# Performance work log

Measured on AMD Instinct MI355X. Metric: run time of the kernel, lower is better.

The kernel has to match this reference:

```python
import jax, jax.numpy as jnp
import numpy as np

B, T, N, C = 4, 2048, 4, 1024   # batch, seq, expansion_rate, hidden_dim
A = 8                            # max_lora_adapters
SINKHORN_ITERS = 20
EPS = 1e-05


def _logit(x):
    x = jnp.clip(x, 1e-06, 1.0 - 1e-06)
    return jnp.log(x) - jnp.log(1.0 - x)


def setup_inputs() -> dict:
    key = jax.random.key(0)
    ks = jax.random.split(key, 12)
    nC = N * C
    x = jax.random.normal(ks[0], (B, T, N, C), dtype=jnp.float32)
    adapter_indices = jax.random.randint(ks[1], (B,), 0, A)
    # Learned parameters (perturbed from the identity init so gradients are non-trivial)
    input_norm_weight = 1.0 + 0.02 * jax.random.normal(ks[2], (A, nC), dtype=jnp.float32)
    phi_pre = 0.02 * jax.random.normal(ks[3], (A, nC, N), dtype=jnp.float32)
    phi_post = 0.02 * jax.random.normal(ks[4], (A, nC, N), dtype=jnp.float32)
    phi_res = 0.02 * jax.random.normal(ks[5], (A, nC, N * N), dtype=jnp.float32)
    b_pre = _logit(jnp.float32(1.0 / N)) + 0.1 * jax.random.normal(ks[6], (A, N), dtype=jnp.float32)
    b_post = 0.1 * jax.random.normal(ks[7], (A, N), dtype=jnp.float32)
    b_res = 10.0 * jnp.eye(N, dtype=jnp.float32) + jax.random.normal(ks[8], (A, N, N), dtype=jnp.float32)
    alpha_pre = 1.0 + 0.1 * jax.random.normal(ks[9], (A,), dtype=jnp.float32)
    alpha_post = 1.0 + 0.1 * jax.random.normal(ks[10], (A,), dtype=jnp.float32)
    alpha_res = 1.0 + 0.1 * jax.random.normal(ks[11], (A,), dtype=jnp.float32)
    return {
        "x": x,
        "input_norm_weight": input_norm_weight,
        "phi_pre": phi_pre, "phi_post": phi_post, "phi_res": phi_res,
        "b_pre": b_pre, "b_post": b_post, "b_res": b_res,
        "alpha_pre": alpha_pre, "alpha_post": alpha_post, "alpha_res": alpha_res,
        "adapter_indices": adapter_indices,
    }


def _sinkhorn_knopp(M, iters):
    M = jnp.exp(M)
    def step(_, mat):
        mat = mat / mat.sum(axis=-1, keepdims=True)
        mat = mat / mat.sum(axis=-2, keepdims=True)
        return mat
    return jax.lax.fori_loop(0, iters, step, M)


def reference(x, input_norm_weight, phi_pre, phi_post, phi_res,
              b_pre, b_post, b_res, alpha_pre, alpha_post, alpha_res,
              adapter_indices):
    Bb, Tt, n, Cc = x.shape
    idx = adapter_indices.astype(jnp.int32)
    x_flat = x.reshape(Bb, Tt, n * Cc)
    # adapter-indexed RMSNorm
    w = input_norm_weight[idx]                                  # [B, nC]
    rms = jnp.sqrt(jnp.mean(x_flat ** 2, axis=-1, keepdims=True) + EPS)
    x_norm = w[:, None, :] * x_flat / rms                       # [B, T, nC]
    # pre: input-dependent aggregation weights H_pre
    pre_logits = jnp.einsum('btd,bdn->btn', x_norm, phi_pre[idx])
    H_pre = jax.nn.sigmoid(alpha_pre[idx][:, None, None] * pre_logits + b_pre[idx][:, None, :])
    x_agg = (H_pre[..., None] * x).sum(axis=-2)                 # [B, T, C]
    output = x_agg                                              # identity block between pre and post
    # post: distribution weights H_post and doubly-stochastic mixing M
    post_logits = jnp.einsum('btd,bdn->btn', x_norm, phi_post[idx])
    H_post = 2.0 * jax.nn.sigmoid(alpha_post[idx][:, None, None] * post_logits + b_post[idx][:, None, :])
    res_logits = jnp.einsum('btd,bdm->btm', x_norm, phi_res[idx]).reshape(Bb, Tt, n, n)
    tilde_H_res = alpha_res[idx][:, None, None, None] * res_logits + b_res[idx][:, None, :, :]
    M = _sinkhorn_knopp(tilde_H_res, SINKHORN_ITERS)            # [B, T, n, n]
    y_dist = H_post[..., None] * output[..., None, :]           # [B, T, n, C]
    x_mixed = jnp.einsum('btij,btjc->btic', M, x)               # [B, T, n, C]
    return x_mixed + y_dist
```

## Files before the change

kernel.cpp:

```cpp
#include <hip/hip_runtime.h>


#define BT 8192
#define NC 4096
#define NC4 1024

__global__ __launch_bounds__(256) void lora_connector_kernel(
    const float* __restrict__ x,
    const float* __restrict__ inw,
    const float* __restrict__ phi_pre,
    const float* __restrict__ phi_post,
    const float* __restrict__ phi_res,
    const float* __restrict__ b_pre,
    const float* __restrict__ b_post,
    const float* __restrict__ b_res,
    const float* __restrict__ alpha_pre,
    const float* __restrict__ alpha_post,
    const float* __restrict__ alpha_res,
    const int*   __restrict__ adapter_indices,
    float* __restrict__ out)
{
    const int tid = threadIdx.x;
    const int g   = tid & 3;
    const int l   = tid >> 2;
    const int wvid= tid >> 6;
    const int ln  = tid & 63;
    const int tok = blockIdx.x * 4 + g;
    const int b   = blockIdx.x >> 9;
    const int idx = adapter_indices[b];

    const float4* __restrict__ x4p = (const float4*)x + (size_t)tok * NC4;
    const float4* __restrict__ w4p = (const float4*)inw + (size_t)idx * NC4;
    const float4* __restrict__ pp4 = (const float4*)(phi_pre  + (size_t)idx * (NC * 4));
    const float4* __restrict__ po4 = (const float4*)(phi_post + (size_t)idx * (NC * 4));
    const float4* __restrict__ pr4 = (const float4*)(phi_res  + (size_t)idx * (NC * 16));

    __shared__ float4 tileL[2][1536];
    __shared__ float red[4][4][26];

    const float4* sg[6];
    int sstr[6];
    #pragma unroll
    for (int i = 0; i < 6; ++i) {
        const int c = wvid * 6 + i;
        const int sp  = ((c & 3) << 6) | ln;
        const int sps = sp ^ ((sp >> 3) & 3);
        const int up  = ((c - 8) << 6) | ln;
        const int ups = up ^ ((up >> 4) & 7);
        const float4* a = (c < 4) ? (pp4 + sps) : (po4 + sps);
        sg[i]   = (c < 8) ? a : (pr4 + ups);
        sstr[i] = (c < 8) ? 256 : 1024;
    }

    #define STAGE_TILE(MT, BF)                                                   \
    {                                                                            \
        _Pragma("unroll")                                                        \
        for (int i = 0; i < 6; ++i) {                                            \
            __builtin_amdgcn_global_load_lds(                                    \
                (const __attribute__((address_space(1))) void*)(sg[i] + (size_t)(MT) * sstr[i]), \
                (__attribute__((address_space(3))) void*)&tileL[BF][(wvid * 6 + i) << 6], \
                16, 0, 0);                                                       \
        }                                                                        \
    }

    STAGE_TILE(0, 0);

    float acc[25];
    #pragma unroll
    for (int j = 0; j < 25; ++j) acc[j] = 0.0f;
    float ssum = 0.0f;

    #pragma unroll 1
    for (int m = 0; m < 16; ++m) {
        const int bf = m & 1;
        __syncthreads();
        if (m < 15) STAGE_TILE(m + 1, bf ^ 1);

        const float4 xv = x4p[m * 64 + l];
        const float4 wv = w4p[m * 64 + l];
        ssum = fmaf(xv.x, xv.x, fmaf(xv.y, xv.y, fmaf(xv.z, xv.z, fmaf(xv.w, xv.w, ssum))));
        const float xw[4] = { xv.x * wv.x, xv.y * wv.y, xv.z * wv.z, xv.w * wv.w };

        #pragma unroll
        for (int e = 0; e < 4; ++e) {
            const float s = xw[e];
            const int sidx = (l << 2) | e;
            const int sswz = sidx ^ ((sidx >> 3) & 3);
            const float4 a = tileL[bf][sswz];
            acc[0] = fmaf(s, a.x, acc[0]); acc[1] = fmaf(s, a.y, acc[1]);
            acc[2] = fmaf(s, a.z, acc[2]); acc[3] = fmaf(s, a.w, acc[3]);
            const float4 p = tileL[bf][256 + sswz];
            acc[4] = fmaf(s, p.x, acc[4]); acc[5] = fmaf(s, p.y, acc[5]);
            acc[6] = fmaf(s, p.z, acc[6]); acc[7] = fmaf(s, p.w, acc[7]);
            #pragma unroll
            for (int q = 0; q < 4; ++q) {
                const int u = (l << 4) | (e << 2) | q;
                const float4 r = tileL[bf][512 + (u ^ ((u >> 4) & 7))];
                acc[8 + q * 4 + 0] = fmaf(s, r.x, acc[8 + q * 4 + 0]);
                acc[8 + q * 4 + 1] = fmaf(s, r.y, acc[8 + q * 4 + 1]);
                acc[8 + q * 4 + 2] = fmaf(s, r.z, acc[8 + q * 4 + 2]);
                acc[8 + q * 4 + 3] = fmaf(s, r.w, acc[8 + q * 4 + 3]);
            }
        }
    }
    acc[24] = ssum;

    #pragma unroll
    for (int j = 0; j < 25; ++j) {
        float v = acc[j];
        v += __shfl_xor(v, 4);
        v += __shfl_xor(v, 8);
        v += __shfl_xor(v, 16);
        v += __shfl_xor(v, 32);
        acc[j] = v;
    }

    __syncthreads();
    if ((ln >> 2) == 0) {
        #pragma unroll
        for (int j = 0; j < 25; ++j) red[wvid][g][j] = acc[j];
    }
    __syncthreads();
    float tot[25];
    #pragma unroll
    for (int j = 0; j < 25; ++j)
        tot[j] = (red[0][g][j] + red[1][g][j]) + (red[2][g][j] + red[3][g][j]);

    const float inv_rms = rsqrtf(tot[24] * (1.0f / 4096.0f) + 1e-5f);
    const float apre  = alpha_pre[idx];
    const float apost = alpha_post[idx];
    const float ares  = alpha_res[idx];

    float Hpre[4], Hpost[4];
    #pragma unroll
    for (int n = 0; n < 4; ++n) {
        const float zp = fmaf(apre,  tot[n]     * inv_rms, b_pre[idx * 4 + n]);
        Hpre[n]  = 1.0f / (1.0f + __expf(-zp));
        const float zq = fmaf(apost, tot[4 + n] * inv_rms, b_post[idx * 4 + n]);
        Hpost[n] = 2.0f / (1.0f + __expf(-zq));
    }

    const int s16 = ln >> 2;
    const int sj = s16 & 3;
    const int si = s16 >> 2;
    float Mv = __expf(fmaf(ares, tot[8 + si * 4 + sj] * inv_rms,
                           b_res[idx * 16 + si * 4 + sj]));
    #pragma unroll
    for (int it = 0; it < 20; ++it) {
        float rs = Mv + __shfl_xor(Mv, 4);
        rs += __shfl_xor(rs, 8);
        Mv *= __builtin_amdgcn_rcpf(rs);
        float cs = Mv + __shfl_xor(Mv, 16);
        cs += __shfl_xor(cs, 32);
        Mv *= __builtin_amdgcn_rcpf(cs);
    }

    float W[4][4];
    #pragma unroll
    for (int ss = 0; ss < 16; ++ss) {
        const float mm = __shfl(Mv, ss * 4 + g);
        W[ss >> 2][ss & 3] = fmaf(Hpost[ss >> 2], Hpre[ss & 3], mm);
    }

    float4* __restrict__ out4 = (float4*)out + (size_t)tok * NC4;
    #pragma unroll
    for (int k = 0; k < 4; ++k) {
        const int c4 = k * 64 + l;
        const float4 x0 = x4p[0 * 256 + c4];
        const float4 x1 = x4p[1 * 256 + c4];
        const float4 x2 = x4p[2 * 256 + c4];
        const float4 x3 = x4p[3 * 256 + c4];
        #pragma unroll
        for (int i = 0; i < 4; ++i) {
            float4 o;
            o.x = fmaf(W[i][0], x0.x, fmaf(W[i][1], x1.x, fmaf(W[i][2], x2.x, W[i][3] * x3.x)));
            o.y = fmaf(W[i][0], x0.y, fmaf(W[i][1], x1.y, fmaf(W[i][2], x2.y, W[i][3] * x3.y)));
            o.z = fmaf(W[i][0], x0.z, fmaf(W[i][1], x1.z, fmaf(W[i][2], x2.z, W[i][3] * x3.z)));
            o.w = fmaf(W[i][0], x0.w, fmaf(W[i][1], x1.w, fmaf(W[i][2], x2.w, W[i][3] * x3.w)));
            out4[i * 256 + c4] = o;
        }
    }
    #undef STAGE_TILE
}

extern "C" void kernel_launch(void* const* d_in, const int* in_sizes, int n_in,
                              void* d_out, int out_size, void* d_ws, size_t ws_size,
                              hipStream_t stream) {
    const float* x         = (const float*)d_in[0];
    const float* inw       = (const float*)d_in[1];
    const float* phi_pre   = (const float*)d_in[2];
    const float* phi_post  = (const float*)d_in[3];
    const float* phi_res   = (const float*)d_in[4];
    const float* b_pre     = (const float*)d_in[5];
    const float* b_post    = (const float*)d_in[6];
    const float* b_res     = (const float*)d_in[7];
    const float* alpha_pre = (const float*)d_in[8];
    const float* alpha_post= (const float*)d_in[9];
    const float* alpha_res = (const float*)d_in[10];
    const int*   adapter   = (const int*)d_in[11];
    float* out = (float*)d_out;

    dim3 grid(BT / 4);
    dim3 block(256);
    lora_connector_kernel<<<grid, block, 0, stream>>>(
        x, inw, phi_pre, phi_post, phi_res,
        b_pre, b_post, b_res,
        alpha_pre, alpha_post, alpha_res,
        adapter, out);
}
```

Measured before the change: 323.9 us.

## Share each phi row across four tokens per thread with register-blocked accumulators

Each thread now owns one column of the hidden dimension and accumulates the projection for all four tokens of the block. Every phi element loaded from LDS is therefore reused four times in registers, which cuts LDS reads per FMA by four and removes the swizzle index math. The x and norm-weight scalars for the next tile are prefetched one iteration ahead. In exchange there are 96+4 accumulators per thread, the occupancy hint is raised to 3, and the cross-lane reduction becomes a transposing butterfly; the scalar global loads of x and weights are also narrower than the previous float4 loads.

Measured after the change: 333.0 us. +2.8%, slower.

```diff
diff --git a/kernel.cpp b/kernel.cpp
--- a/kernel.cpp
+++ b/kernel.cpp
@@ -5,7 +5,7 @@
 #define NC 4096
 #define NC4 1024
 
-__global__ __launch_bounds__(256) void lora_connector_kernel(
+__global__ __launch_bounds__(256, 3) void lora_connector_kernel(
     const float* __restrict__ x,
     const float* __restrict__ inw,
     const float* __restrict__ phi_pre,
@@ -25,15 +25,15 @@
     const int l   = tid >> 2;
     const int wvid= tid >> 6;
     const int ln  = tid & 63;
-    const int tok = blockIdx.x * 4 + g;
-    const int b   = blockIdx.x >> 9;
+    const int blk = blockIdx.x;
+    const int b   = blk >> 9;
     const int idx = adapter_indices[b];
 
-    const float4* __restrict__ x4p = (const float4*)x + (size_t)tok * NC4;
-    const float4* __restrict__ w4p = (const float4*)inw + (size_t)idx * NC4;
     const float4* __restrict__ pp4 = (const float4*)(phi_pre  + (size_t)idx * (NC * 4));
     const float4* __restrict__ po4 = (const float4*)(phi_post + (size_t)idx * (NC * 4));
     const float4* __restrict__ pr4 = (const float4*)(phi_res  + (size_t)idx * (NC * 16));
+    const float*  __restrict__ inwp = inw + (size_t)idx * NC + tid;
+    const float*  __restrict__ xb   = x + (size_t)(blk * 4) * NC + tid;
 
     __shared__ float4 tileL[2][1536];
     __shared__ float red[4][4][26];
@@ -43,13 +43,19 @@
     #pragma unroll
     for (int i = 0; i < 6; ++i) {
         const int c = wvid * 6 + i;
-        const int sp  = ((c & 3) << 6) | ln;
-        const int sps = sp ^ ((sp >> 3) & 3);
-        const int up  = ((c - 8) << 6) | ln;
-        const int ups = up ^ ((up >> 4) & 7);
-        const float4* a = (c < 4) ? (pp4 + sps) : (po4 + sps);
-        sg[i]   = (c < 8) ? a : (pr4 + ups);
-        sstr[i] = (c < 8) ? 256 : 1024;
+        const float4* bp; int off, str;
+        if (c < 8) {
+            bp  = (c < 4) ? pp4 : po4;
+            off = ((c & 3) << 6) + ln;
+            str = 256;
+        } else {
+            const int k = c - 8;
+            bp  = pr4;
+            off = ((((k & 3) << 6) + ln) << 2) + (k >> 2);
+            str = 1024;
+        }
+        sg[i] = bp + off;
+        sstr[i] = str;
     }
 
     #define STAGE_TILE(MT, BF)                                                   \
@@ -65,10 +71,18 @@
 
     STAGE_TILE(0, 0);
 
-    float acc[25];
-    #pragma unroll
-    for (int j = 0; j < 25; ++j) acc[j] = 0.0f;
-    float ssum = 0.0f;
+    float acc[24][4];
+    float ss[4];
+    #pragma unroll
+    for (int j = 0; j < 24; ++j) {
+        acc[j][0] = 0.0f; acc[j][1] = 0.0f; acc[j][2] = 0.0f; acc[j][3] = 0.0f;
+    }
+    ss[0] = ss[1] = ss[2] = ss[3] = 0.0f;
+
+    float xn[4], wn;
+    #pragma unroll
+    for (int j = 0; j < 4; ++j) xn[j] = xb[j * NC];
+    wn = inwp[0];
 
     #pragma unroll 1
     for (int m = 0; m < 16; ++m) {
@@ -76,52 +90,76 @@
         __syncthreads();
         if (m < 15) STAGE_TILE(m + 1, bf ^ 1);
 
-        const float4 xv = x4p[m * 64 + l];
-        const float4 wv = w4p[m * 64 + l];
-        ssum = fmaf(xv.x, xv.x, fmaf(xv.y, xv.y, fmaf(xv.z, xv.z, fmaf(xv.w, xv.w, ssum))));
-        const float xw[4] = { xv.x * wv.x, xv.y * wv.y, xv.z * wv.z, xv.w * wv.w };
-
-        #pragma unroll
-        for (int e = 0; e < 4; ++e) {
-            const float s = xw[e];
-            const int sidx = (l << 2) | e;
-            const int sswz = sidx ^ ((sidx >> 3) & 3);
-            const float4 a = tileL[bf][sswz];
-            acc[0] = fmaf(s, a.x, acc[0]); acc[1] = fmaf(s, a.y, acc[1]);
-            acc[2] = fmaf(s, a.z, acc[2]); acc[3] = fmaf(s, a.w, acc[3]);
-            const float4 p = tileL[bf][256 + sswz];
-            acc[4] = fmaf(s, p.x, acc[4]); acc[5] = fmaf(s, p.y, acc[5]);
-            acc[6] = fmaf(s, p.z, acc[6]); acc[7] = fmaf(s, p.w, acc[7]);
+        const float wv = wn;
+        float s[4];
+        #pragma unroll
+        for (int j = 0; j < 4; ++j) {
+            const float xv = xn[j];
+            s[j] = xv * wv;
+            ss[j] = fmaf(xv, xv, ss[j]);
+        }
+        if (m < 15) {
             #pragma unroll
-            for (int q = 0; q < 4; ++q) {
-                const int u = (l << 4) | (e << 2) | q;
-                const float4 r = tileL[bf][512 + (u ^ ((u >> 4) & 7))];
-                acc[8 + q * 4 + 0] = fmaf(s, r.x, acc[8 + q * 4 + 0]);
-                acc[8 + q * 4 + 1] = fmaf(s, r.y, acc[8 + q * 4 + 1]);
-                acc[8 + q * 4 + 2] = fmaf(s, r.z, acc[8 + q * 4 + 2]);
-                acc[8 + q * 4 + 3] = fmaf(s, r.w, acc[8 + q * 4 + 3]);
+            for (int j = 0; j < 4; ++j) xn[j] = xb[j * NC + (m + 1) * 256];
+            wn = inwp[(m + 1) * 256];
+        }
+
+        const float4 a = tileL[bf][tid];
+        #pragma unroll
+        for (int j = 0; j < 4; ++j) {
+            acc[0][j] = fmaf(s[j], a.x, acc[0][j]);
+            acc[1][j] = fmaf(s[j], a.y, acc[1][j]);
+            acc[2][j] = fmaf(s[j], a.z, acc[2][j]);
+            acc[3][j] = fmaf(s[j], a.w, acc[3][j]);
+        }
+        const float4 p = tileL[bf][256 + tid];
+        #pragma unroll
+        for (int j = 0; j < 4; ++j) {
+            acc[4][j] = fmaf(s[j], p.x, acc[4][j]);
+            acc[5][j] = fmaf(s[j], p.y, acc[5][j]);
+            acc[6][j] = fmaf(s[j], p.z, acc[6][j]);
+            acc[7][j] = fmaf(s[j], p.w, acc[7][j]);
+        }
+        #pragma unroll
+        for (int q = 0; q < 4; ++q) {
+            const float4 r = tileL[bf][512 + q * 256 + tid];
+            #pragma unroll
+            for (int j = 0; j < 4; ++j) {
+                acc[8 + q * 4 + 0][j] = fmaf(s[j], r.x, acc[8 + q * 4 + 0][j]);
+                acc[8 + q * 4 + 1][j] = fmaf(s[j], r.y, acc[8 + q * 4 + 1][j]);
+                acc[8 + q * 4 + 2][j] = fmaf(s[j], r.z, acc[8 + q * 4 + 2][j]);
+                acc[8 + q * 4 + 3][j] = fmaf(s[j], r.w, acc[8 + q * 4 + 3][j]);
             }
         }
     }
-    acc[24] = ssum;
-
-    #pragma unroll
-    for (int j = 0; j < 25; ++j) {
-        float v = acc[j];
-        v += __shfl_xor(v, 4);
-        v += __shfl_xor(v, 8);
-        v += __shfl_xor(v, 16);
-        v += __shfl_xor(v, 32);
-        acc[j] = v;
-    }
-
+
+    float tot[25];
+    #define RED4(V0, V1, V2, V3, DST)                                   \
+    {                                                                   \
+        const float u0 = (V0) + __shfl_xor((V0), 1);                    \
+        const float u1 = (V1) + __shfl_xor((V1), 1);                    \
+        const float u2 = (V2) + __shfl_xor((V2), 1);                    \
+        const float u3 = (V3) + __shfl_xor((V3), 1);                    \
+        const float r0 = (ln & 1) ? u1 : u0;                            \
+        const float r1 = (ln & 1) ? u3 : u2;                            \
+        const float w0 = r0 + __shfl_xor(r0, 2);                        \
+        const float w1 = r1 + __shfl_xor(r1, 2);                        \
+        float tv = (ln & 2) ? w1 : w0;                                  \
+        tv += __shfl_xor(tv, 4);  tv += __shfl_xor(tv, 8);              \
+        tv += __shfl_xor(tv, 16); tv += __shfl_xor(tv, 32);             \
+        (DST) = tv;                                                     \
+    }
+    #pragma unroll
+    for (int j = 0; j < 24; ++j)
+        RED4(acc[j][0], acc[j][1], acc[j][2], acc[j][3], tot[j]);
+    RED4(ss[0], ss[1], ss[2], ss[3], tot[24]);
+    #undef RED4
+
+    if (ln < 4) {
+        #pragma unroll
+        for (int j = 0; j < 25; ++j) red[wvid][ln][j] = tot[j];
+    }
     __syncthreads();
-    if ((ln >> 2) == 0) {
-        #pragma unroll
-        for (int j = 0; j < 25; ++j) red[wvid][g][j] = acc[j];
-    }
-    __syncthreads();
-    float tot[25];
     #pragma unroll
     for (int j = 0; j < 25; ++j)
         tot[j] = (red[0][g][j] + red[1][g][j]) + (red[2][g][j] + red[3][g][j]);
@@ -157,11 +195,13 @@
 
     float W[4][4];
     #pragma unroll
-    for (int ss = 0; ss < 16; ++ss) {
-        const float mm = __shfl(Mv, ss * 4 + g);
-        W[ss >> 2][ss & 3] = fmaf(Hpost[ss >> 2], Hpre[ss & 3], mm);
-    }
-
+    for (int sq = 0; sq < 16; ++sq) {
+        const float mm = __shfl(Mv, sq * 4 + g);
+        W[sq >> 2][sq & 3] = fmaf(Hpost[sq >> 2], Hpre[sq & 3], mm);
+    }
+
+    const int tok = blk * 4 + g;
+    const float4* __restrict__ x4p = (const float4*)x + (size_t)tok * NC4;
     float4* __restrict__ out4 = (float4*)out + (size_t)tok * NC4;
     #pragma unroll
     for (int k = 0; k < 4; ++k) {
```
